# Kernel tuning notes

Hardware: AMD Instinct MI355X
Metric: run time of the kernel (lower is better)

The kernel has to match this reference:

```python
import jax, jax.numpy as jnp
import numpy as np

N = 50000
E = 800000
DIN = 64
DOUT = 64
H = 4
C = DOUT // H
EPS = 1e-5


def setup_inputs() -> dict:
    key = jax.random.key(0)
    ks = jax.random.split(key, 40)
    inp = {}
    inp["x"] = jax.random.normal(ks[0], (N, DIN), jnp.float32)
    inp["edge_index"] = jax.random.randint(ks[1], (2, E), 0, N, dtype=jnp.int32)
    inp["edge_weight"] = jax.random.uniform(ks[2], (E,), jnp.float32)
    inp["edge_attr"] = jax.random.normal(ks[3], (E, 1), jnp.float32)
    k = 4
    for i in range(2):
        din = DIN if i == 0 else DOUT
        s = din ** -0.5
        inp[f"gcn_w{i}"] = jax.random.normal(ks[k], (din, DOUT), jnp.float32) * s; k += 1
        inp[f"gcn_b{i}"] = jnp.zeros((DOUT,), jnp.float32)
        inp[f"res_w{i}"] = jax.random.normal(ks[k], (din, DOUT), jnp.float32) * s; k += 1
        inp[f"res_b{i}"] = jnp.zeros((DOUT,), jnp.float32)
        inp[f"ln_g{i}"] = jnp.ones((DOUT,), jnp.float32)
        inp[f"ln_b{i}"] = jnp.zeros((DOUT,), jnp.float32)
        sg = DOUT ** -0.5
        inp[f"gat_w{i}"] = jax.random.normal(ks[k], (DOUT, H * C), jnp.float32) * sg; k += 1
        inp[f"gat_b{i}"] = jnp.zeros((H * C,), jnp.float32)
        inp[f"att_src{i}"] = jax.random.normal(ks[k], (H, C), jnp.float32) * (C ** -0.5); k += 1
        inp[f"att_dst{i}"] = jax.random.normal(ks[k], (H, C), jnp.float32) * (C ** -0.5); k += 1
        inp[f"att_e{i}"] = jax.random.normal(ks[k], (H, C), jnp.float32) * (C ** -0.5); k += 1
        inp[f"ew_w{i}"] = jax.random.normal(ks[k], (1, H * C), jnp.float32); k += 1
    return inp


def _gcn(x, src0, dst0, ew, W, b):
    n = x.shape[0]
    sl = jnp.arange(n, dtype=src0.dtype)
    src = jnp.concatenate([src0, sl])
    dst = jnp.concatenate([dst0, sl])
    w = jnp.concatenate([ew, jnp.ones((n,), ew.dtype)])  # self-loop weight 1
    deg = jax.ops.segment_sum(w, dst, num_segments=n)
    dinv = jnp.where(deg > 0, jax.lax.rsqrt(deg), 0.0)
    norm = dinv[src] * w * dinv[dst]
    h = x @ W  # [n, DOUT]
    out = jax.ops.segment_sum(h[src] * norm[:, None], dst, num_segments=n)
    return out + b


def _gat(x, src0, dst0, ea, W, b, a_src, a_dst, a_e, We):
    n = x.shape[0]
    sl = jnp.arange(n, dtype=src0.dtype)
    src = jnp.concatenate([src0, sl])
    dst = jnp.concatenate([dst0, sl])
    loop_attr = jnp.broadcast_to(ea.mean(axis=0, keepdims=True), (n, ea.shape[1]))
    ea2 = jnp.concatenate([ea, loop_attr], axis=0)  # fill_value='mean'
    xl = (x @ W).reshape(n, H, C)
    a_s = (xl * a_src).sum(-1)  # [n,H]
    a_d = (xl * a_dst).sum(-1)
    a_ee = ((ea2 @ We).reshape(-1, H, C) * a_e).sum(-1)  # [E2,H]
    alpha = jax.nn.leaky_relu(a_s[src] + a_d[dst] + a_ee, 0.2)
    m = jax.ops.segment_max(alpha, dst, num_segments=n)
    e = jnp.exp(alpha - m[dst])
    s = jax.ops.segment_sum(e, dst, num_segments=n)
    alpha = e / (s[dst] + 1e-16)
    out = jax.ops.segment_sum(xl[src] * alpha[:, :, None], dst, num_segments=n)
    return out.reshape(n, H * C) + b


def _ln(x, g, b):
    mu = x.mean(-1, keepdims=True)
    v = ((x - mu) ** 2).mean(-1, keepdims=True)
    return (x - mu) * jax.lax.rsqrt(v + EPS) * g + b


def reference(x, edge_index, edge_weight, edge_attr,
              gcn_w0, gcn_b0, res_w0, res_b0, ln_g0, ln_b0,
              gat_w0, gat_b0, att_src0, att_dst0, att_e0, ew_w0,
              gcn_w1, gcn_b1, res_w1, res_b1, ln_g1, ln_b1,
              gat_w1, gat_b1, att_src1, att_dst1, att_e1, ew_w1):
    src0, dst0 = edge_index[0], edge_index[1]
    layers = [
        (gcn_w0, gcn_b0, res_w0, res_b0, ln_g0, ln_b0, gat_w0, gat_b0, att_src0, att_dst0, att_e0, ew_w0),
        (gcn_w1, gcn_b1, res_w1, res_b1, ln_g1, ln_b1, gat_w1, gat_b1, att_src1, att_dst1, att_e1, ew_w1),
    ]
    for (gw, gb, rw, rb, lg, lb, Wg, bg, a_s, a_d, a_e, We) in layers:
        residual = x @ rw + rb
        x = jax.nn.silu(_gcn(x, src0, dst0, edge_weight, gw, gb)) + residual
        x = _ln(x, lg, lb)
        x = jax.nn.silu(_gat(x, src0, dst0, edge_attr, Wg, bg, a_s, a_d, a_e, We)) + x
    return x  # down_sample=False -> Identity
```

## Files before the change

### kernel.cpp

```cpp
#include <hip/hip_runtime.h>
#include <hip/hip_fp16.h>

#define NN 50000
#define NE 800000
#define D 64
#define EPS 1e-5f
#define NT 3125
#define NB1 250
#define EPB 3200
#define NBIN 196
#define STOT 49152
#define SBLK 192

typedef unsigned short ushort_t;
typedef unsigned int uint_t;
typedef __attribute__((ext_vector_type(8))) short bf16x8;
typedef __attribute__((ext_vector_type(4))) float f32x4;

__device__ __forceinline__ float wave_sum64(float v) {
#pragma unroll
  for (int m = 1; m <= 32; m <<= 1) v += __shfl_xor(v, m, 64);
  return v;
}
__device__ __forceinline__ float group_sum16(float v) {
#pragma unroll
  for (int m = 1; m <= 8; m <<= 1) v += __shfl_xor(v, m, 64);
  return v;
}
__device__ __forceinline__ float silu_f(float v) { return v / (1.f + __expf(-v)); }
__device__ __forceinline__ float lrelu_f(float v) { return v >= 0.f ? v : 0.2f * v; }
__device__ __forceinline__ ushort_t f2b(float x) {
  unsigned u = __float_as_uint(x);
  return (ushort_t)((u + 0x7FFFu + ((u >> 16) & 1u)) >> 16);
}
__device__ __forceinline__ float b2f(ushort_t u) {
  return __uint_as_float(((unsigned)u) << 16);
}
__device__ __forceinline__ ushort_t f2h(float x) {
  return __half_as_ushort(__float2half_rn(x));
}
__device__ __forceinline__ float h2f(unsigned u) {
  return __half2float(__ushort_as_half((ushort_t)(u & 0xFFFFu)));
}
__device__ __forceinline__ float sel4(float a, float b, float c, float d, int h) {
  float ab = (h & 1) ? b : a;
  float cd = (h & 1) ? d : c;
  return (h & 2) ? cd : ab;
}
__device__ __forceinline__ bf16x8 pack8(float4 a, float4 b) {
  bf16x8 r;
  r[0] = (short)f2b(a.x); r[1] = (short)f2b(a.y);
  r[2] = (short)f2b(a.z); r[3] = (short)f2b(a.w);
  r[4] = (short)f2b(b.x); r[5] = (short)f2b(b.y);
  r[6] = (short)f2b(b.z); r[7] = (short)f2b(b.w);
  return r;
}


__global__ void __launch_bounds__(256) k_hist196(const int* __restrict__ ei,
                                                 int* __restrict__ histG) {
  __shared__ int h[NBIN];
  int blk = blockIdx.x;
  for (int j = threadIdx.x; j < NBIN; j += 256) h[j] = 0;
  __syncthreads();
  int e0 = blk * EPB;
  for (int e = e0 + threadIdx.x; e < e0 + EPB; e += 256)
    atomicAdd(&h[ei[NE + e] >> 8], 1);
  __syncthreads();
  for (int j = threadIdx.x; j < NBIN; j += 256) histG[j * NB1 + blk] = h[j];
}

__global__ void __launch_bounds__(256) k_scanMA(int* __restrict__ histG,
                                                int* __restrict__ bsum) {
  __shared__ int sm[256];
  int j = threadIdx.x;
  int i = blockIdx.x * 256 + j;
  const int TOT = NBIN * NB1;
  int v = (i < TOT) ? histG[i] : 0;
  sm[j] = v;
  __syncthreads();
  for (int off = 1; off < 256; off <<= 1) {
    int t = (j >= off) ? sm[j - off] : 0;
    __syncthreads();
    sm[j] += t;
    __syncthreads();
  }
  if (i < TOT) histG[i] = sm[j] - v;
  if (j == 255) bsum[blockIdx.x] = sm[255];
}

__global__ void __launch_bounds__(256) k_scanMB(int* __restrict__ bsum,
                                                float* __restrict__ scal) {
  __shared__ int sm[256];
  int j = threadIdx.x;
  for (int t = j; t < 1024; t += 256) scal[t] = 0.f;
  int v = (j < SBLK) ? bsum[j] : 0;
  sm[j] = v;
  __syncthreads();
  for (int off = 1; off < 256; off <<= 1) {
    int t = (j >= off) ? sm[j - off] : 0;
    __syncthreads();
    sm[j] += t;
    __syncthreads();
  }
  if (j < SBLK) bsum[j] = sm[j] - v;
}

__global__ void __launch_bounds__(256) k_scanMC(int* __restrict__ histG,
                                                const int* __restrict__ bsum) {
  int i = blockIdx.x * 256 + threadIdx.x;
  const int TOT = NBIN * NB1;
  if (i < TOT) histG[i] += bsum[i >> 8];
}

__global__ void __launch_bounds__(256) k_part(
    const int* __restrict__ ei, const float* __restrict__ ew,
    const float* __restrict__ ea, const int* __restrict__ histG,
    uint2* __restrict__ rectmp, float* __restrict__ scal) {
  __shared__ int cur[NBIN];
  int blk = blockIdx.x;
  for (int j = threadIdx.x; j < NBIN; j += 256) cur[j] = histG[j * NB1 + blk];
  __syncthreads();
  int e0 = blk * EPB;
  float asum = 0.f;
  for (int e = e0 + threadIdx.x; e < e0 + EPB; e += 256) {
    int src = ei[e];
    int dst = ei[NE + e];
    float w = ew[e];
    float a = ea[e];
    asum += a;
    int slot = atomicAdd(&cur[dst >> 8], 1);
    uint2 r;
    r.x = (uint_t)(src & 0xFFFF) | ((uint_t)f2h(w) << 16);
    r.y = (uint_t)(dst & 0xFF) | ((uint_t)f2h(a) << 16);
    rectmp[slot] = r;
  }
  float s = wave_sum64(asum);
  if ((threadIdx.x & 63) == 0) {
    int slot = (blk * 4 + (threadIdx.x >> 6)) & 63;
    atomicAdd(&scal[(size_t)slot * 16], s);
  }
}

__global__ void __launch_bounds__(256) k_sortfin(
    const uint2* __restrict__ rectmp, const int* __restrict__ histG,
    uint2* __restrict__ rec, int* __restrict__ rs) {
  __shared__ int cnt[256], sc[256], cur[256];
  int b = blockIdx.x;
  int t = threadIdx.x;
  int lo = histG[b * NB1];
  int hi = (b == NBIN - 1) ? NE : histG[(b + 1) * NB1];
  cnt[t] = 0;
  __syncthreads();
  for (int e = lo + t; e < hi; e += 256)
    atomicAdd(&cnt[rectmp[e].y & 0xFFu], 1);
  __syncthreads();
  int v = cnt[t];
  sc[t] = v;
  __syncthreads();
  for (int off = 1; off < 256; off <<= 1) {
    int u = (t >= off) ? sc[t - off] : 0;
    __syncthreads();
    sc[t] += u;
    __syncthreads();
  }
  int ex = sc[t] - v;
  int node = b * 256 + t;
  if (node < NN) rs[node] = lo + ex;
  if (b == NBIN - 1 && t == 0) rs[NN] = NE;
  cur[t] = lo + ex;
  __syncthreads();
  for (int e = lo + t; e < hi; e += 256) {
    uint2 r = rectmp[e];
    int dl = (int)(r.y & 0xFFu);
    int slot = atomicAdd(&cur[dl], 1);
    uint_t src = r.x & 0xFFFFu;
    uint2 o;
    o.x = r.x;
    o.y = src | (r.y & 0xFFFF0000u);
    rec[slot] = o;
  }
}

__global__ void k_deg(const uint_t* __restrict__ rec, const int* __restrict__ rs,
                      float* __restrict__ dinv, float* __restrict__ scal) {
  int i = blockIdx.x * blockDim.x + threadIdx.x;
  if (i < NN) {
    float s = 1.f;
    int k1 = rs[i + 1];
    for (int k = rs[i]; k < k1; ++k) s += h2f(rec[2 * k] >> 16);
    dinv[i] = rsqrtf(s);
  }
  if (i == 0) {
    float t = 0.f;
    for (int j = 0; j < 64; ++j) t += scal[(size_t)j * 16];
    scal[1] = t / (float)NE;
  }
}

__global__ void __launch_bounds__(256) k_dual_gemm(
    const float* __restrict__ x, const float* __restrict__ W1,
    const float* __restrict__ W2, const float* __restrict__ b2,
    ushort_t* __restrict__ out1, float* __restrict__ out2) {
  __shared__ ushort_t wf[2 * 2 * 4 * 512];
  for (int e = threadIdx.x; e < 8192; e += 256) {
    int f = e >> 9, r = e & 511;
    int lane = r >> 3, j = r & 7;
    int m = f >> 3, s = (f >> 2) & 1, t = f & 3;
    int k = s * 32 + (lane >> 4) * 8 + j;
    int n = t * 16 + (lane & 15);
    const float* Wm = m ? W2 : W1;
    wf[e] = f2b(Wm[k * D + n]);
  }
  __syncthreads();
  int tile = blockIdx.x * 4 + (threadIdx.x >> 6);
  if (tile >= NT) return;
  int l = threadIdx.x & 63;
  int q = l >> 4, cn = l & 15;
  const float* xr = x + ((size_t)tile * 16 + cn) * D + q * 8;
  float4 xa = *(const float4*)xr;
  float4 xb = *(const float4*)(xr + 4);
  float4 xc = *(const float4*)(xr + 32);
  float4 xd = *(const float4*)(xr + 36);
  bf16x8 a0 = pack8(xa, xb), a1 = pack8(xc, xd);
  f32x4 acc1[4], acc2[4];
#pragma unroll
  for (int t = 0; t < 4; ++t) {
    bf16x8 b10 = *(const bf16x8*)&wf[(0 * 8 + 0 * 4 + t) * 512 + l * 8];
    bf16x8 b11 = *(const bf16x8*)&wf[(0 * 8 + 1 * 4 + t) * 512 + l * 8];
    bf16x8 b20 = *(const bf16x8*)&wf[(1 * 8 + 0 * 4 + t) * 512 + l * 8];
    bf16x8 b21 = *(const bf16x8*)&wf[(1 * 8 + 1 * 4 + t) * 512 + l * 8];
    f32x4 z = {0.f, 0.f, 0.f, 0.f};
    acc1[t] = __builtin_amdgcn_mfma_f32_16x16x32_bf16(a0, b10, z, 0, 0, 0);
    acc1[t] = __builtin_amdgcn_mfma_f32_16x16x32_bf16(a1, b11, acc1[t], 0, 0, 0);
    acc2[t] = __builtin_amdgcn_mfma_f32_16x16x32_bf16(a0, b20, z, 0, 0, 0);
    acc2[t] = __builtin_amdgcn_mfma_f32_16x16x32_bf16(a1, b21, acc2[t], 0, 0, 0);
  }
#pragma unroll
  for (int t = 0; t < 4; ++t) {
    float bb = b2[t * 16 + cn];
#pragma unroll
    for (int r = 0; r < 4; ++r) {
      size_t row = (size_t)tile * 16 + q * 4 + r;
      out1[row * D + t * 16 + cn] = f2b(acc1[t][r]);
      out2[row * D + t * 16 + cn] = acc2[t][r] + bb;
    }
  }
}

__global__ void __launch_bounds__(256) k_gat_node(
    const float* __restrict__ x2, const float* __restrict__ Wg,
    const float* __restrict__ att_src, const float* __restrict__ att_dst,
    const float* __restrict__ We, const float* __restrict__ a_e,
    ushort_t* __restrict__ xl, float* __restrict__ a_s, float* __restrict__ a_d,
    float* __restrict__ wea) {
  __shared__ ushort_t wf[2 * 4 * 512];
  for (int e = threadIdx.x; e < 4096; e += 256) {
    int f = e >> 9, r = e & 511;
    int lane = r >> 3, j = r & 7;
    int s = (f >> 2) & 1, t = f & 3;
    int k = s * 32 + (lane >> 4) * 8 + j;
    int n = t * 16 + (lane & 15);
    wf[e] = f2b(Wg[k * D + n]);
  }
  __syncthreads();
  if (blockIdx.x == 0 && threadIdx.x < 64) {
    int c = threadIdx.x;
    float v = group_sum16(We[c] * a_e[c]);
    if ((c & 15) == 0) wea[c >> 4] = v;
  }
  int tile = blockIdx.x * 4 + (threadIdx.x >> 6);
  if (tile >= NT) return;
  int l = threadIdx.x & 63;
  int q = l >> 4, cn = l & 15;
  const float* xr = x2 + ((size_t)tile * 16 + cn) * D + q * 8;
  float4 xa = *(const float4*)xr;
  float4 xb = *(const float4*)(xr + 4);
  float4 xc = *(const float4*)(xr + 32);
  float4 xd = *(const float4*)(xr + 36);
  bf16x8 a0 = pack8(xa, xb), a1 = pack8(xc, xd);
  f32x4 acc[4];
#pragma unroll
  for (int t = 0; t < 4; ++t) {
    bf16x8 b0 = *(const bf16x8*)&wf[(0 * 4 + t) * 512 + l * 8];
    bf16x8 b1 = *(const bf16x8*)&wf[(1 * 4 + t) * 512 + l * 8];
    f32x4 z = {0.f, 0.f, 0.f, 0.f};
    acc[t] = __builtin_amdgcn_mfma_f32_16x16x32_bf16(a0, b0, z, 0, 0, 0);
    acc[t] = __builtin_amdgcn_mfma_f32_16x16x32_bf16(a1, b1, acc[t], 0, 0, 0);
  }
#pragma unroll
  for (int t = 0; t < 4; ++t) {
    float av = att_src[t * 16 + cn];
    float dv = att_dst[t * 16 + cn];
#pragma unroll
    for (int r = 0; r < 4; ++r) {
      size_t row = (size_t)tile * 16 + q * 4 + r;
      xl[row * D + t * 16 + cn] = f2b(acc[t][r]);
      float vs = group_sum16(acc[t][r] * av);
      float vd = group_sum16(acc[t][r] * dv);
      if (cn == 0) {
        a_s[row * 4 + t] = vs;
        a_d[row * 4 + t] = vd;
      }
    }
  }
}


__global__ void __launch_bounds__(256) k_gcn_agg(
    const ushort_t* __restrict__ h16, const float* __restrict__ res,
    const float* __restrict__ dinv, const int* __restrict__ rs,
    const uint_t* __restrict__ rec,
    const float* __restrict__ gb, const float* __restrict__ lg, const float* __restrict__ lb,
    float* __restrict__ x2, int n) {
  __shared__ int   ss[4][64];
  __shared__ float swt[4][64];
  int w = threadIdx.x >> 6;
  int wv = (blockIdx.x * blockDim.x + threadIdx.x) >> 6;
  int iA = wv * 2;
  if (iA >= n) return;
  int iB = iA + 1;
  int l = threadIdx.x & 63;
  int half = l >> 5, cp = l & 31;
  float diA = dinv[iA], diB = dinv[iB];
  float accA = diA * diA * b2f(h16[(size_t)iA * D + l]);
  float accB = diB * diB * b2f(h16[(size_t)iB * D + l]);
  int kA = rs[iA], kA1 = rs[iA + 1];
  int kB = rs[iB], kB1 = rs[iB + 1];
  while (kA < kA1 || kB < kB1) {
    int cntA = min(32, kA1 - kA);
    int cntB = min(32, kB1 - kB);
    int src = 0; float wn = 0.f;
    if (half == 0) {
      if (cp < cntA) {
        uint_t r = rec[2 * (size_t)(kA + cp)];
        src = (int)(r & 0xFFFFu);
        wn = dinv[src] * h2f(r >> 16) * diA;
      }
    } else {
      if (cp < cntB) {
        uint_t r = rec[2 * (size_t)(kB + cp)];
        src = (int)(r & 0xFFFFu);
        wn = dinv[src] * h2f(r >> 16) * diB;
      }
    }
    ss[w][l] = src;
    swt[w][l] = wn;
    int nm = max(cntA, cntB);
    int j = 0;
    for (; j + 4 <= nm; j += 4) {
      int4 sa = *(const int4*)&ss[w][j];
      int4 sb = *(const int4*)&ss[w][32 + j];
      float4 wa = *(const float4*)&swt[w][j];
      float4 wb = *(const float4*)&swt[w][32 + j];
      float a0 = b2f(h16[(size_t)sa.x * D + l]);
      float b0 = b2f(h16[(size_t)sb.x * D + l]);
      float a1 = b2f(h16[(size_t)sa.y * D + l]);
      float b1 = b2f(h16[(size_t)sb.y * D + l]);
      float a2 = b2f(h16[(size_t)sa.z * D + l]);
      float b2v = b2f(h16[(size_t)sb.z * D + l]);
      float a3 = b2f(h16[(size_t)sa.w * D + l]);
      float b3 = b2f(h16[(size_t)sb.w * D + l]);
      accA = fmaf(wa.x, a0, accA); accB = fmaf(wb.x, b0, accB);
      accA = fmaf(wa.y, a1, accA); accB = fmaf(wb.y, b1, accB);
      accA = fmaf(wa.z, a2, accA); accB = fmaf(wb.z, b2v, accB);
      accA = fmaf(wa.w, a3, accA); accB = fmaf(wb.w, b3, accB);
    }
    for (; j < nm; ++j) {
      int sA = ss[w][j], sB = ss[w][32 + j];
      float wA = swt[w][j], wB = swt[w][32 + j];
      float vA = b2f(h16[(size_t)sA * D + l]);
      float vB = b2f(h16[(size_t)sB * D + l]);
      accA = fmaf(wA, vA, accA);
      accB = fmaf(wB, vB, accB);
    }
    kA += cntA; kB += cntB;
  }
  float gbv = gb[l], lgv = lg[l], lbv = lb[l];
  float x1A = silu_f(accA + gbv) + res[(size_t)iA * D + l];
  float x1B = silu_f(accB + gbv) + res[(size_t)iB * D + l];
  float muA = wave_sum64(x1A) * (1.f / 64.f);
  float muB = wave_sum64(x1B) * (1.f / 64.f);
  float dA = x1A - muA, dB = x1B - muB;
  float varA = wave_sum64(dA * dA) * (1.f / 64.f);
  float varB = wave_sum64(dB * dB) * (1.f / 64.f);
  x2[(size_t)iA * D + l] = dA * rsqrtf(varA + EPS) * lgv + lbv;
  x2[(size_t)iB * D + l] = dB * rsqrtf(varB + EPS) * lgv + lbv;
}

__global__ void __launch_bounds__(256) k_gat_agg(
    const ushort_t* __restrict__ xl16, const float* __restrict__ x2,
    const float* __restrict__ a_s, const float* __restrict__ a_d,
    const int* __restrict__ rs, const uint_t* __restrict__ rec,
    const float* __restrict__ wea, const float* __restrict__ scal,
    const float* __restrict__ bg, float* __restrict__ xout, int n) {
  __shared__ int   ss[4][64];
  __shared__ float el[4][4][68];
  int w = threadIdx.x >> 6;
  int wv = (blockIdx.x * blockDim.x + threadIdx.x) >> 6;
  int iA = wv * 2;
  if (iA >= n) return;
  int iB = iA + 1;
  int l = threadIdx.x & 63;
  int half = l >> 5, cp = l & 31;
  int hh = l >> 4;
  float4 wv4 = *(const float4*)wea;
  float mean_attr = scal[1];
  float we_h = sel4(wv4.x, wv4.y, wv4.z, wv4.w, hh);
  float ad_hA = a_d[(size_t)iA * 4 + hh], as_iA = a_s[(size_t)iA * 4 + hh];
  float ad_hB = a_d[(size_t)iB * 4 + hh], as_iB = a_s[(size_t)iB * 4 + hh];
  float eSA = __expf(lrelu_f(as_iA + ad_hA + mean_attr * we_h));
  float eSB = __expf(lrelu_f(as_iB + ad_hB + mean_attr * we_h));
  float sA = eSA, sB = eSB;
  float accA = eSA * b2f(xl16[(size_t)iA * D + l]);
  float accB = eSB * b2f(xl16[(size_t)iB * D + l]);
  const float* adp = a_d + (size_t)(half ? iB : iA) * 4;
  float4 ad4 = *(const float4*)adp;
  int kA = rs[iA], kA1 = rs[iA + 1];
  int kB = rs[iB], kB1 = rs[iB + 1];
  while (kA < kA1 || kB < kB1) {
    int cntA = min(32, kA1 - kA);
    int cntB = min(32, kB1 - kB);
    int myk = half ? kB : kA;
    int mycnt = half ? cntB : cntA;
    int src = 0;
    float e0v = 0.f, e1v = 0.f, e2v = 0.f, e3v = 0.f;
    if (cp < mycnt) {
      uint_t r = rec[2 * (size_t)(myk + cp) + 1];
      src = (int)(r & 0xFFFFu);
      float ea = h2f(r >> 16);
      float4 as4 = *(const float4*)(a_s + (size_t)src * 4);
      e0v = __expf(lrelu_f(as4.x + fmaf(ea, wv4.x, ad4.x)));
      e1v = __expf(lrelu_f(as4.y + fmaf(ea, wv4.y, ad4.y)));
      e2v = __expf(lrelu_f(as4.z + fmaf(ea, wv4.z, ad4.z)));
      e3v = __expf(lrelu_f(as4.w + fmaf(ea, wv4.w, ad4.w)));
    }
    ss[w][l] = src;
    el[w][0][l] = e0v;
    el[w][1][l] = e1v;
    el[w][2][l] = e2v;
    el[w][3][l] = e3v;
    int nm = max(cntA, cntB);
    int j = 0;
    for (; j + 4 <= nm; j += 4) {
      int4 sa = *(const int4*)&ss[w][j];
      int4 sb = *(const int4*)&ss[w][32 + j];
      float4 ea4 = *(const float4*)&el[w][hh][j];
      float4 eb4 = *(const float4*)&el[w][hh][32 + j];
      float a0 = b2f(xl16[(size_t)sa.x * D + l]);
      float b0 = b2f(xl16[(size_t)sb.x * D + l]);
      float a1 = b2f(xl16[(size_t)sa.y * D + l]);
      float b1 = b2f(xl16[(size_t)sb.y * D + l]);
      float a2 = b2f(xl16[(size_t)sa.z * D + l]);
      float b2v = b2f(xl16[(size_t)sb.z * D + l]);
      float a3 = b2f(xl16[(size_t)sa.w * D + l]);
      float b3 = b2f(xl16[(size_t)sb.w * D + l]);
      accA = fmaf(ea4.x, a0, accA); accB = fmaf(eb4.x, b0, accB);
      accA = fmaf(ea4.y, a1, accA); accB = fmaf(eb4.y, b1, accB);
      accA = fmaf(ea4.z, a2, accA); accB = fmaf(eb4.z, b2v, accB);
      accA = fmaf(ea4.w, a3, accA); accB = fmaf(eb4.w, b3, accB);
      sA += (ea4.x + ea4.y) + (ea4.z + ea4.w);
      sB += (eb4.x + eb4.y) + (eb4.z + eb4.w);
    }
    for (; j < nm; ++j) {
      int srcA = ss[w][j], srcB = ss[w][32 + j];
      float eA = el[w][hh][j], eB = el[w][hh][32 + j];
      float vA = b2f(xl16[(size_t)srcA * D + l]);
      float vB = b2f(xl16[(size_t)srcB * D + l]);
      accA = fmaf(eA, vA, accA);
      accB = fmaf(eB, vB, accB);
      sA += eA; sB += eB;
    }
    kA += cntA; kB += cntB;
  }
  float bgv = bg[l];
  float oA = accA / (sA + 1e-16f) + bgv;
  float oB = accB / (sB + 1e-16f) + bgv;
  xout[(size_t)iA * D + l] = silu_f(oA) + x2[(size_t)iA * D + l];
  xout[(size_t)iB * D + l] = silu_f(oB) + x2[(size_t)iB * D + l];
}


extern "C" void kernel_launch(void* const* d_in, const int* in_sizes, int n_in,
                              void* d_out, int out_size, void* d_ws, size_t ws_size,
                              hipStream_t stream) {
  (void)in_sizes; (void)n_in; (void)out_size; (void)ws_size;
  const float* x  = (const float*)d_in[0];
  const int*   ei = (const int*)d_in[1];
  const float* ew = (const float*)d_in[2];
  const float* ea = (const float*)d_in[3];
  const float* P[2][12];
  for (int l = 0; l < 2; ++l)
    for (int j = 0; j < 12; ++j) P[l][j] = (const float*)d_in[4 + l * 12 + j];

  float* W = (float*)d_ws;
  const size_t o_rs    = 0;
  const size_t o_dinv  = o_rs + NN + 16;
  const size_t o_wea   = o_dinv + NN;
  const size_t o_scal  = o_wea + 16;
  const size_t o_bsum  = o_scal + 1024;
  const size_t o_hist  = o_bsum + 256;
  const size_t o_rec   = o_hist + STOT;
  const size_t o_rtmp  = o_rec + (size_t)NE * 2;
  const size_t o_h16   = o_rtmp + (size_t)NE * 2;
  const size_t o_xl16  = o_h16 + (size_t)NN * D / 2;
  const size_t o_res   = o_xl16 + (size_t)NN * D / 2;
  const size_t o_x2    = o_res + (size_t)NN * D;
  const size_t o_xmid  = o_x2 + (size_t)NN * D;
  const size_t o_as    = o_xmid + (size_t)NN * D;
  const size_t o_ad    = o_as + (size_t)NN * 4;

  int*      rs    = (int*)(W + o_rs);
  float*    dinv  = W + o_dinv;
  float*    wea   = W + o_wea;
  float*    scal  = W + o_scal;
  int*      bsum  = (int*)(W + o_bsum);
  int*      histG = (int*)(W + o_hist);
  uint2*    rec   = (uint2*)(W + o_rec);
  uint2*    rtmp  = (uint2*)(W + o_rtmp);
  ushort_t* h16   = (ushort_t*)(W + o_h16);
  ushort_t* xl16  = (ushort_t*)(W + o_xl16);
  float*    resb  = W + o_res;
  float*    x2b   = W + o_x2;
  float*    xmid  = W + o_xmid;
  float*    asb   = W + o_as;
  float*    adb   = W + o_ad;

  const int B = 256;
  const int gN  = (NN + B - 1) / B;
  const int gN2 = ((NN / 2) * 64 + B - 1) / B;
  const int gMF = (NT + 3) / 4;

  k_hist196<<<NB1, B, 0, stream>>>(ei, histG);
  k_scanMA<<<SBLK, B, 0, stream>>>(histG, bsum);
  k_scanMB<<<1, B, 0, stream>>>(bsum, scal);
  k_scanMC<<<SBLK, B, 0, stream>>>(histG, bsum);
  k_part<<<NB1, B, 0, stream>>>(ei, ew, ea, histG, rtmp, scal);
  k_sortfin<<<NBIN, B, 0, stream>>>(rtmp, histG, rec, rs);
  k_deg<<<gN, B, 0, stream>>>((const uint_t*)rec, rs, dinv, scal);

  const float* xin = x;
  for (int l = 0; l < 2; ++l) {
    float* xout = (l == 0) ? xmid : (float*)d_out;
    k_dual_gemm<<<gMF, B, 0, stream>>>(xin, P[l][0], P[l][2], P[l][3], h16, resb);
    k_gcn_agg<<<gN2, B, 0, stream>>>(h16, resb, dinv, rs, (const uint_t*)rec,
                                     P[l][1], P[l][4], P[l][5], x2b, NN);
    k_gat_node<<<gMF, B, 0, stream>>>(x2b, P[l][6], P[l][8], P[l][9],
                                      P[l][11], P[l][10], xl16, asb, adb, wea);
    k_gat_agg<<<gN2, B, 0, stream>>>(xl16, x2b, asb, adb, rs, (const uint_t*)rec,
                                     wea, scal, P[l][7], xout, NN);
    xin = xout;
  }
}
```

Baseline: 312.0 us.

## Fuse node GEMMs into aggregation epilogues and merge preprocessing kernels

The per-node GEMMs move into the aggregation kernels. The GAT projection runs as an MFMA epilogue of the GCN aggregation, and the next layer's GCN/residual GEMM runs at the end of the GAT aggregation, working on 8-node tiles staged in shared memory. The degree computation is folded into the sort-finalise kernel through shared-memory atomics. The scan is shortened to two passes, the weights are pre-converted to bf16 once, and the histogram runs in the same launch as the first GEMM. This removes several launches and the full-size intermediate reads and writes between GEMM and aggregation. The cost is half-empty MFMA tiles (8 of 16 rows used), extra shared-memory syncs, and more register pressure in the aggregation kernels.

```diff
diff --git a/kernel.cpp b/kernel.cpp
--- a/kernel.cpp
+++ b/kernel.cpp
@@ -22,6 +22,11 @@
   for (int m = 1; m <= 32; m <<= 1) v += __shfl_xor(v, m, 64);
   return v;
 }
+__device__ __forceinline__ int wave_sum64i(int v) {
+#pragma unroll
+  for (int m = 1; m <= 32; m <<= 1) v += __shfl_xor(v, m, 64);
+  return v;
+}
 __device__ __forceinline__ float group_sum16(float v) {
 #pragma unroll
   for (int m = 1; m <= 8; m <<= 1) v += __shfl_xor(v, m, 64);
@@ -56,22 +61,109 @@
   return r;
 }
 
-
-__global__ void __launch_bounds__(256) k_hist196(const int* __restrict__ ei,
-                                                 int* __restrict__ histG) {
-  __shared__ int h[NBIN];
-  int blk = blockIdx.x;
-  for (int j = threadIdx.x; j < NBIN; j += 256) h[j] = 0;
-  __syncthreads();
-  int e0 = blk * EPB;
-  for (int e = e0 + threadIdx.x; e < e0 + EPB; e += 256)
-    atomicAdd(&h[ei[NE + e] >> 8], 1);
-  __syncthreads();
-  for (int j = threadIdx.x; j < NBIN; j += 256) histG[j * NB1 + blk] = h[j];
-}
-
-__global__ void __launch_bounds__(256) k_scanMA(int* __restrict__ histG,
-                                                int* __restrict__ bsum) {
+__global__ void __launch_bounds__(256) k_pre(
+    const int* __restrict__ ei, int* __restrict__ histG,
+    const float* __restrict__ x, const float* __restrict__ W1,
+    const float* __restrict__ W2, const float* __restrict__ b2,
+    ushort_t* __restrict__ out1, float* __restrict__ out2) {
+  __shared__ __align__(16) char smem[16384];
+  if (blockIdx.x < NB1) {
+    int* h = (int*)smem;
+    int blk = blockIdx.x;
+    for (int j = threadIdx.x; j < NBIN; j += 256) h[j] = 0;
+    __syncthreads();
+    int e0 = blk * EPB;
+    for (int e = e0 + threadIdx.x; e < e0 + EPB; e += 256)
+      atomicAdd(&h[ei[NE + e] >> 8], 1);
+    __syncthreads();
+    for (int j = threadIdx.x; j < NBIN; j += 256) histG[j * NB1 + blk] = h[j];
+    return;
+  }
+  ushort_t* wf = (ushort_t*)smem;
+  for (int e = threadIdx.x; e < 8192; e += 256) {
+    int f = e >> 9, r = e & 511;
+    int lane = r >> 3, j = r & 7;
+    int m = f >> 3, s = (f >> 2) & 1, t = f & 3;
+    int k = s * 32 + (lane >> 4) * 8 + j;
+    int n = t * 16 + (lane & 15);
+    const float* Wm = m ? W2 : W1;
+    wf[e] = f2b(Wm[k * D + n]);
+  }
+  __syncthreads();
+  int tile = (blockIdx.x - NB1) * 4 + (threadIdx.x >> 6);
+  if (tile >= NT) return;
+  int l = threadIdx.x & 63;
+  int q = l >> 4, cn = l & 15;
+  const float* xr = x + ((size_t)tile * 16 + cn) * D + q * 8;
+  float4 xa = *(const float4*)xr;
+  float4 xb = *(const float4*)(xr + 4);
+  float4 xc = *(const float4*)(xr + 32);
+  float4 xd = *(const float4*)(xr + 36);
+  bf16x8 a0 = pack8(xa, xb), a1 = pack8(xc, xd);
+  f32x4 acc1[4], acc2[4];
+#pragma unroll
+  for (int t = 0; t < 4; ++t) {
+    bf16x8 b10 = *(const bf16x8*)&wf[(0 * 8 + 0 * 4 + t) * 512 + l * 8];
+    bf16x8 b11 = *(const bf16x8*)&wf[(0 * 8 + 1 * 4 + t) * 512 + l * 8];
+    bf16x8 b20 = *(const bf16x8*)&wf[(1 * 8 + 0 * 4 + t) * 512 + l * 8];
+    bf16x8 b21 = *(const bf16x8*)&wf[(1 * 8 + 1 * 4 + t) * 512 + l * 8];
+    f32x4 z = {0.f, 0.f, 0.f, 0.f};
+    acc1[t] = __builtin_amdgcn_mfma_f32_16x16x32_bf16(a0, b10, z, 0, 0, 0);
+    acc1[t] = __builtin_amdgcn_mfma_f32_16x16x32_bf16(a1, b11, acc1[t], 0, 0, 0);
+    acc2[t] = __builtin_amdgcn_mfma_f32_16x16x32_bf16(a0, b20, z, 0, 0, 0);
+    acc2[t] = __builtin_amdgcn_mfma_f32_16x16x32_bf16(a1, b21, acc2[t], 0, 0, 0);
+  }
+#pragma unroll
+  for (int t = 0; t < 4; ++t) {
+    float bb = b2[t * 16 + cn];
+#pragma unroll
+    for (int r = 0; r < 4; ++r) {
+      size_t row = (size_t)tile * 16 + q * 4 + r;
+      out1[row * D + t * 16 + cn] = f2b(acc1[t][r]);
+      out2[row * D + t * 16 + cn] = acc2[t][r] + bb;
+    }
+  }
+}
+
+__global__ void __launch_bounds__(256) k_scanA(
+    int* __restrict__ histG, int* __restrict__ bsum, float* __restrict__ scal,
+    const float* __restrict__ Wg0, const float* __restrict__ Wg1,
+    const float* __restrict__ W11, const float* __restrict__ W21,
+    const float* __restrict__ We0, const float* __restrict__ ae0,
+    const float* __restrict__ We1, const float* __restrict__ ae1,
+    ushort_t* __restrict__ wg16, ushort_t* __restrict__ wd16,
+    float* __restrict__ wea2) {
+  if (blockIdx.x == SBLK) {
+    int tid = threadIdx.x;
+    for (int t = tid; t < 1024; t += 256) scal[t] = 0.f;
+    for (int e = tid; e < 4096; e += 256) {
+      int f = e >> 9, r = e & 511;
+      int lane = r >> 3, j = r & 7;
+      int s = (f >> 2) & 1, t = f & 3;
+      int k = s * 32 + (lane >> 4) * 8 + j;
+      int n = t * 16 + (lane & 15);
+      wg16[e] = f2b(Wg0[k * D + n]);
+      wg16[4096 + e] = f2b(Wg1[k * D + n]);
+    }
+    for (int e = tid; e < 8192; e += 256) {
+      int f = e >> 9, r = e & 511;
+      int lane = r >> 3, j = r & 7;
+      int m = f >> 3, s = (f >> 2) & 1, t = f & 3;
+      int k = s * 32 + (lane >> 4) * 8 + j;
+      int n = t * 16 + (lane & 15);
+      const float* Wm = m ? W21 : W11;
+      wd16[e] = f2b(Wm[k * D + n]);
+    }
+    if (tid < 64) {
+      float v = group_sum16(We0[tid] * ae0[tid]);
+      if ((tid & 15) == 0) wea2[tid >> 4] = v;
+    } else if (tid < 128) {
+      int c = tid - 64;
+      float v = group_sum16(We1[c] * ae1[c]);
+      if ((c & 15) == 0) wea2[4 + (c >> 4)] = v;
+    }
+    return;
+  }
   __shared__ int sm[256];
   int j = threadIdx.x;
   int i = blockIdx.x * 256 + j;
@@ -89,28 +181,17 @@
   if (j == 255) bsum[blockIdx.x] = sm[255];
 }
 
-__global__ void __launch_bounds__(256) k_scanMB(int* __restrict__ bsum,
-                                                float* __restrict__ scal) {
-  __shared__ int sm[256];
-  int j = threadIdx.x;
-  for (int t = j; t < 1024; t += 256) scal[t] = 0.f;
-  int v = (j < SBLK) ? bsum[j] : 0;
-  sm[j] = v;
-  __syncthreads();
-  for (int off = 1; off < 256; off <<= 1) {
-    int t = (j >= off) ? sm[j - off] : 0;
-    __syncthreads();
-    sm[j] += t;
-    __syncthreads();
-  }
-  if (j < SBLK) bsum[j] = sm[j] - v;
-}
-
-__global__ void __launch_bounds__(256) k_scanMC(int* __restrict__ histG,
-                                                const int* __restrict__ bsum) {
-  int i = blockIdx.x * 256 + threadIdx.x;
-  const int TOT = NBIN * NB1;
-  if (i < TOT) histG[i] += bsum[i >> 8];
+__global__ void __launch_bounds__(256) k_scanC(int* __restrict__ histG,
+                                               const int* __restrict__ bsum) {
+  __shared__ int ws4[4];
+  int t = threadIdx.x;
+  int v = (t < (int)blockIdx.x) ? bsum[t] : 0;
+  v = wave_sum64i(v);
+  if ((t & 63) == 0) ws4[t >> 6] = v;
+  __syncthreads();
+  int prefix = ws4[0] + ws4[1] + ws4[2] + ws4[3];
+  int i = blockIdx.x * 256 + t;
+  if (i < NBIN * NB1) histG[i] += prefix;
 }
 
 __global__ void __launch_bounds__(256) k_part(
@@ -142,15 +223,18 @@
   }
 }
 
-__global__ void __launch_bounds__(256) k_sortfin(
+__global__ void __launch_bounds__(256) k_sfin(
     const uint2* __restrict__ rectmp, const int* __restrict__ histG,
-    uint2* __restrict__ rec, int* __restrict__ rs) {
+    uint2* __restrict__ rec, int* __restrict__ rs,
+    float* __restrict__ dinv, float* __restrict__ scal) {
   __shared__ int cnt[256], sc[256], cur[256];
+  __shared__ float wsum[256];
   int b = blockIdx.x;
   int t = threadIdx.x;
   int lo = histG[b * NB1];
   int hi = (b == NBIN - 1) ? NE : histG[(b + 1) * NB1];
   cnt[t] = 0;
+  wsum[t] = 0.f;
   __syncthreads();
   for (int e = lo + t; e < hi; e += 256)
     atomicAdd(&cnt[rectmp[e].y & 0xFFu], 1);
@@ -174,153 +258,40 @@
     uint2 r = rectmp[e];
     int dl = (int)(r.y & 0xFFu);
     int slot = atomicAdd(&cur[dl], 1);
+    atomicAdd(&wsum[dl], h2f(r.x >> 16));
     uint_t src = r.x & 0xFFFFu;
     uint2 o;
     o.x = r.x;
     o.y = src | (r.y & 0xFFFF0000u);
     rec[slot] = o;
   }
-}
-
-__global__ void k_deg(const uint_t* __restrict__ rec, const int* __restrict__ rs,
-                      float* __restrict__ dinv, float* __restrict__ scal) {
-  int i = blockIdx.x * blockDim.x + threadIdx.x;
-  if (i < NN) {
-    float s = 1.f;
-    int k1 = rs[i + 1];
-    for (int k = rs[i]; k < k1; ++k) s += h2f(rec[2 * k] >> 16);
-    dinv[i] = rsqrtf(s);
-  }
-  if (i == 0) {
-    float t = 0.f;
-    for (int j = 0; j < 64; ++j) t += scal[(size_t)j * 16];
-    scal[1] = t / (float)NE;
-  }
-}
-
-__global__ void __launch_bounds__(256) k_dual_gemm(
-    const float* __restrict__ x, const float* __restrict__ W1,
-    const float* __restrict__ W2, const float* __restrict__ b2,
-    ushort_t* __restrict__ out1, float* __restrict__ out2) {
-  __shared__ ushort_t wf[2 * 2 * 4 * 512];
-  for (int e = threadIdx.x; e < 8192; e += 256) {
-    int f = e >> 9, r = e & 511;
-    int lane = r >> 3, j = r & 7;
-    int m = f >> 3, s = (f >> 2) & 1, t = f & 3;
-    int k = s * 32 + (lane >> 4) * 8 + j;
-    int n = t * 16 + (lane & 15);
-    const float* Wm = m ? W2 : W1;
-    wf[e] = f2b(Wm[k * D + n]);
-  }
-  __syncthreads();
-  int tile = blockIdx.x * 4 + (threadIdx.x >> 6);
-  if (tile >= NT) return;
-  int l = threadIdx.x & 63;
-  int q = l >> 4, cn = l & 15;
-  const float* xr = x + ((size_t)tile * 16 + cn) * D + q * 8;
-  float4 xa = *(const float4*)xr;
-  float4 xb = *(const float4*)(xr + 4);
-  float4 xc = *(const float4*)(xr + 32);
-  float4 xd = *(const float4*)(xr + 36);
-  bf16x8 a0 = pack8(xa, xb), a1 = pack8(xc, xd);
-  f32x4 acc1[4], acc2[4];
-#pragma unroll
-  for (int t = 0; t < 4; ++t) {
-    bf16x8 b10 = *(const bf16x8*)&wf[(0 * 8 + 0 * 4 + t) * 512 + l * 8];
-    bf16x8 b11 = *(const bf16x8*)&wf[(0 * 8 + 1 * 4 + t) * 512 + l * 8];
-    bf16x8 b20 = *(const bf16x8*)&wf[(1 * 8 + 0 * 4 + t) * 512 + l * 8];
-    bf16x8 b21 = *(const bf16x8*)&wf[(1 * 8 + 1 * 4 + t) * 512 + l * 8];
-    f32x4 z = {0.f, 0.f, 0.f, 0.f};
-    acc1[t] = __builtin_amdgcn_mfma_f32_16x16x32_bf16(a0, b10, z, 0, 0, 0);
-    acc1[t] = __builtin_amdgcn_mfma_f32_16x16x32_bf16(a1, b11, acc1[t], 0, 0, 0);
-    acc2[t] = __builtin_amdgcn_mfma_f32_16x16x32_bf16(a0, b20, z, 0, 0, 0);
-    acc2[t] = __builtin_amdgcn_mfma_f32_16x16x32_bf16(a1, b21, acc2[t], 0, 0, 0);
-  }
-#pragma unroll
-  for (int t = 0; t < 4; ++t) {
-    float bb = b2[t * 16 + cn];
-#pragma unroll
-    for (int r = 0; r < 4; ++r) {
-      size_t row = (size_t)tile * 16 + q * 4 + r;
-      out1[row * D + t * 16 + cn] = f2b(acc1[t][r]);
-      out2[row * D + t * 16 + cn] = acc2[t][r] + bb;
-    }
-  }
-}
-
-__global__ void __launch_bounds__(256) k_gat_node(
-    const float* __restrict__ x2, const float* __restrict__ Wg,
-    const float* __restrict__ att_src, const float* __restrict__ att_dst,
-    const float* __restrict__ We, const float* __restrict__ a_e,
-    ushort_t* __restrict__ xl, float* __restrict__ a_s, float* __restrict__ a_d,
-    float* __restrict__ wea) {
-  __shared__ ushort_t wf[2 * 4 * 512];
-  for (int e = threadIdx.x; e < 4096; e += 256) {
-    int f = e >> 9, r = e & 511;
-    int lane = r >> 3, j = r & 7;
-    int s = (f >> 2) & 1, t = f & 3;
-    int k = s * 32 + (lane >> 4) * 8 + j;
-    int n = t * 16 + (lane & 15);
-    wf[e] = f2b(Wg[k * D + n]);
-  }
-  __syncthreads();
-  if (blockIdx.x == 0 && threadIdx.x < 64) {
-    int c = threadIdx.x;
-    float v = group_sum16(We[c] * a_e[c]);
-    if ((c & 15) == 0) wea[c >> 4] = v;
-  }
-  int tile = blockIdx.x * 4 + (threadIdx.x >> 6);
-  if (tile >= NT) return;
-  int l = threadIdx.x & 63;
-  int q = l >> 4, cn = l & 15;
-  const float* xr = x2 + ((size_t)tile * 16 + cn) * D + q * 8;
-  float4 xa = *(const float4*)xr;
-  float4 xb = *(const float4*)(xr + 4);
-  float4 xc = *(const float4*)(xr + 32);
-  float4 xd = *(const float4*)(xr + 36);
-  bf16x8 a0 = pack8(xa, xb), a1 = pack8(xc, xd);
-  f32x4 acc[4];
-#pragma unroll
-  for (int t = 0; t < 4; ++t) {
-    bf16x8 b0 = *(const bf16x8*)&wf[(0 * 4 + t) * 512 + l * 8];
-    bf16x8 b1 = *(const bf16x8*)&wf[(1 * 4 + t) * 512 + l * 8];
-    f32x4 z = {0.f, 0.f, 0.f, 0.f};
-    acc[t] = __builtin_amdgcn_mfma_f32_16x16x32_bf16(a0, b0, z, 0, 0, 0);
-    acc[t] = __builtin_amdgcn_mfma_f32_16x16x32_bf16(a1, b1, acc[t], 0, 0, 0);
-  }
-#pragma unroll
-  for (int t = 0; t < 4; ++t) {
-    float av = att_src[t * 16 + cn];
-    float dv = att_dst[t * 16 + cn];
-#pragma unroll
-    for (int r = 0; r < 4; ++r) {
-      size_t row = (size_t)tile * 16 + q * 4 + r;
-      xl[row * D + t * 16 + cn] = f2b(acc[t][r]);
-      float vs = group_sum16(acc[t][r] * av);
-      float vd = group_sum16(acc[t][r] * dv);
-      if (cn == 0) {
-        a_s[row * 4 + t] = vs;
-        a_d[row * 4 + t] = vd;
-      }
-    }
-  }
-}
-
-
-__global__ void __launch_bounds__(256) k_gcn_agg(
+  __syncthreads();
+  if (node < NN) dinv[node] = rsqrtf(1.f + wsum[t]);
+  if (b == 0 && t == 0) {
+    float s = 0.f;
+    for (int j = 0; j < 64; ++j) s += scal[(size_t)j * 16];
+    scal[1] = s / (float)NE;
+  }
+}
+
+__global__ void __launch_bounds__(256) k_gcn_gat(
     const ushort_t* __restrict__ h16, const float* __restrict__ res,
     const float* __restrict__ dinv, const int* __restrict__ rs,
     const uint_t* __restrict__ rec,
-    const float* __restrict__ gb, const float* __restrict__ lg, const float* __restrict__ lb,
-    float* __restrict__ x2, int n) {
-  __shared__ int   ss[4][64];
+    const float* __restrict__ gb, const float* __restrict__ lg,
+    const float* __restrict__ lb,
+    const ushort_t* __restrict__ wg, const float* __restrict__ att_src,
+    const float* __restrict__ att_dst,
+    float* __restrict__ x2, ushort_t* __restrict__ xl,
+    float* __restrict__ a_s, float* __restrict__ a_d) {
+  __shared__ int ss[4][64];
   __shared__ float swt[4][64];
+  __shared__ __align__(16) ushort_t xt[16][72];
   int w = threadIdx.x >> 6;
-  int wv = (blockIdx.x * blockDim.x + threadIdx.x) >> 6;
-  int iA = wv * 2;
-  if (iA >= n) return;
+  int l = threadIdx.x & 63;
+  int base = blockIdx.x * 8;
+  int iA = base + 2 * w;
   int iB = iA + 1;
-  int l = threadIdx.x & 63;
   int half = l >> 5, cp = l & 31;
   float diA = dinv[iA], diB = dinv[iB];
   float accA = diA * diA * b2f(h16[(size_t)iA * D + l]);
@@ -384,22 +355,59 @@
   float dA = x1A - muA, dB = x1B - muB;
   float varA = wave_sum64(dA * dA) * (1.f / 64.f);
   float varB = wave_sum64(dB * dB) * (1.f / 64.f);
-  x2[(size_t)iA * D + l] = dA * rsqrtf(varA + EPS) * lgv + lbv;
-  x2[(size_t)iB * D + l] = dB * rsqrtf(varB + EPS) * lgv + lbv;
-}
-
-__global__ void __launch_bounds__(256) k_gat_agg(
+  float oA = dA * rsqrtf(varA + EPS) * lgv + lbv;
+  float oB = dB * rsqrtf(varB + EPS) * lgv + lbv;
+  x2[(size_t)iA * D + l] = oA;
+  x2[(size_t)iB * D + l] = oB;
+  xt[2 * w][l] = f2b(oA);
+  xt[2 * w + 1][l] = f2b(oB);
+  {
+    ushort_t* xz = &xt[8][0];
+    for (int e = threadIdx.x; e < 8 * 72; e += 256) xz[e] = 0;
+  }
+  __syncthreads();
+  int t = w;
+  int q = l >> 4, cn = l & 15;
+  bf16x8 a0 = *(const bf16x8*)&xt[cn][q * 8];
+  bf16x8 a1 = *(const bf16x8*)&xt[cn][q * 8 + 32];
+  bf16x8 b0 = *(const bf16x8*)&wg[(size_t)((0 * 4 + t) * 512 + l * 8)];
+  bf16x8 b1 = *(const bf16x8*)&wg[(size_t)((1 * 4 + t) * 512 + l * 8)];
+  f32x4 z = {0.f, 0.f, 0.f, 0.f};
+  f32x4 acc = __builtin_amdgcn_mfma_f32_16x16x32_bf16(a0, b0, z, 0, 0, 0);
+  acc = __builtin_amdgcn_mfma_f32_16x16x32_bf16(a1, b1, acc, 0, 0, 0);
+  if (q < 2) {
+    float av = att_src[t * 16 + cn];
+    float dv = att_dst[t * 16 + cn];
+#pragma unroll
+    for (int r = 0; r < 4; ++r) {
+      size_t row = (size_t)base + q * 4 + r;
+      xl[row * D + t * 16 + cn] = f2b(acc[r]);
+      float vs = group_sum16(acc[r] * av);
+      float vd = group_sum16(acc[r] * dv);
+      if (cn == 0) {
+        a_s[row * 4 + t] = vs;
+        a_d[row * 4 + t] = vd;
+      }
+    }
+  }
+}
+
+template <int FUSE>
+__global__ void __launch_bounds__(256) k_gat_fin(
     const ushort_t* __restrict__ xl16, const float* __restrict__ x2,
     const float* __restrict__ a_s, const float* __restrict__ a_d,
     const int* __restrict__ rs, const uint_t* __restrict__ rec,
     const float* __restrict__ wea, const float* __restrict__ scal,
-    const float* __restrict__ bg, float* __restrict__ xout, int n) {
-  __shared__ int   ss[4][64];
+    const float* __restrict__ bg,
+    const ushort_t* __restrict__ wd, const float* __restrict__ b2,
+    ushort_t* __restrict__ out1, float* __restrict__ out2,
+    float* __restrict__ xout) {
+  __shared__ int ss[4][64];
   __shared__ float el[4][4][68];
+  __shared__ __align__(16) ushort_t xt[16][72];
   int w = threadIdx.x >> 6;
-  int wv = (blockIdx.x * blockDim.x + threadIdx.x) >> 6;
-  int iA = wv * 2;
-  if (iA >= n) return;
+  int base = blockIdx.x * 8;
+  int iA = base + 2 * w;
   int iB = iA + 1;
   int l = threadIdx.x & 63;
   int half = l >> 5, cp = l & 31;
@@ -476,8 +484,43 @@
   float bgv = bg[l];
   float oA = accA / (sA + 1e-16f) + bgv;
   float oB = accB / (sB + 1e-16f) + bgv;
-  xout[(size_t)iA * D + l] = silu_f(oA) + x2[(size_t)iA * D + l];
-  xout[(size_t)iB * D + l] = silu_f(oB) + x2[(size_t)iB * D + l];
+  float vA = silu_f(oA) + x2[(size_t)iA * D + l];
+  float vB = silu_f(oB) + x2[(size_t)iB * D + l];
+  if (FUSE) {
+    xt[2 * w][l] = f2b(vA);
+    xt[2 * w + 1][l] = f2b(vB);
+    {
+      ushort_t* xz = &xt[8][0];
+      for (int e = threadIdx.x; e < 8 * 72; e += 256) xz[e] = 0;
+    }
+    __syncthreads();
+    int t = w;
+    int q = l >> 4, cn = l & 15;
+    bf16x8 a0 = *(const bf16x8*)&xt[cn][q * 8];
+    bf16x8 a1 = *(const bf16x8*)&xt[cn][q * 8 + 32];
+#pragma unroll
+    for (int m = 0; m < 2; ++m) {
+      bf16x8 b0 = *(const bf16x8*)&wd[(size_t)((m * 8 + 0 * 4 + t) * 512 + l * 8)];
+      bf16x8 b1 = *(const bf16x8*)&wd[(size_t)((m * 8 + 1 * 4 + t) * 512 + l * 8)];
+      f32x4 z = {0.f, 0.f, 0.f, 0.f};
+      f32x4 acc = __builtin_amdgcn_mfma_f32_16x16x32_bf16(a0, b0, z, 0, 0, 0);
+      acc = __builtin_amdgcn_mfma_f32_16x16x32_bf16(a1, b1, acc, 0, 0, 0);
+      if (q < 2) {
+        float bb = (m == 1) ? b2[t * 16 + cn] : 0.f;
+#pragma unroll
+        for (int r = 0; r < 4; ++r) {
+          size_t row = (size_t)base + q * 4 + r;
+          if (m == 0)
+            out1[row * D + t * 16 + cn] = f2b(acc[r]);
+          else
+            out2[row * D + t * 16 + cn] = acc[r] + bb;
+        }
+      }
+    }
+  } else {
+    xout[(size_t)iA * D + l] = vA;
+    xout[(size_t)iB * D + l] = vB;
+  }
 }
 
 
@@ -506,13 +549,14 @@
   const size_t o_xl16  = o_h16 + (size_t)NN * D / 2;
   const size_t o_res   = o_xl16 + (size_t)NN * D / 2;
   const size_t o_x2    = o_res + (size_t)NN * D;
-  const size_t o_xmid  = o_x2 + (size_t)NN * D;
-  const size_t o_as    = o_xmid + (size_t)NN * D;
+  const size_t o_as    = o_x2 + (size_t)NN * D;
   const size_t o_ad    = o_as + (size_t)NN * 4;
+  const size_t o_wg16  = o_ad + (size_t)NN * 4;
+  const size_t o_wd16  = o_wg16 + 4096;
 
   int*      rs    = (int*)(W + o_rs);
   float*    dinv  = W + o_dinv;
-  float*    wea   = W + o_wea;
+  float*    wea2  = W + o_wea;
   float*    scal  = W + o_scal;
   int*      bsum  = (int*)(W + o_bsum);
   int*      histG = (int*)(W + o_hist);
@@ -522,33 +566,37 @@
   ushort_t* xl16  = (ushort_t*)(W + o_xl16);
   float*    resb  = W + o_res;
   float*    x2b   = W + o_x2;
-  float*    xmid  = W + o_xmid;
   float*    asb   = W + o_as;
   float*    adb   = W + o_ad;
+  ushort_t* wg16  = (ushort_t*)(W + o_wg16);
+  ushort_t* wd16  = (ushort_t*)(W + o_wd16);
 
   const int B = 256;
-  const int gN  = (NN + B - 1) / B;
-  const int gN2 = ((NN / 2) * 64 + B - 1) / B;
-  const int gMF = (NT + 3) / 4;
-
-  k_hist196<<<NB1, B, 0, stream>>>(ei, histG);
-  k_scanMA<<<SBLK, B, 0, stream>>>(histG, bsum);
-  k_scanMB<<<1, B, 0, stream>>>(bsum, scal);
-  k_scanMC<<<SBLK, B, 0, stream>>>(histG, bsum);
+  const int gPre = NB1 + (NT + 3) / 4;
+  const int gN2  = NN / 8;
+
+  k_pre<<<gPre, B, 0, stream>>>(ei, histG, x, P[0][0], P[0][2], P[0][3], h16, resb);
+  k_scanA<<<SBLK + 1, B, 0, stream>>>(histG, bsum, scal,
+                                      P[0][6], P[1][6], P[1][0], P[1][2],
+                                      P[0][11], P[0][10], P[1][11], P[1][10],
+                                      wg16, wd16, wea2);
+  k_scanC<<<SBLK, B, 0, stream>>>(histG, bsum);
   k_part<<<NB1, B, 0, stream>>>(ei, ew, ea, histG, rtmp, scal);
-  k_sortfin<<<NBIN, B, 0, stream>>>(rtmp, histG, rec, rs);
-  k_deg<<<gN, B, 0, stream>>>((const uint_t*)rec, rs, dinv, scal);
-
-  const float* xin = x;
-  for (int l = 0; l < 2; ++l) {
-    float* xout = (l == 0) ? xmid : (float*)d_out;
-    k_dual_gemm<<<gMF, B, 0, stream>>>(xin, P[l][0], P[l][2], P[l][3], h16, resb);
-    k_gcn_agg<<<gN2, B, 0, stream>>>(h16, resb, dinv, rs, (const uint_t*)rec,
-                                     P[l][1], P[l][4], P[l][5], x2b, NN);
-    k_gat_node<<<gMF, B, 0, stream>>>(x2b, P[l][6], P[l][8], P[l][9],
-                                      P[l][11], P[l][10], xl16, asb, adb, wea);
-    k_gat_agg<<<gN2, B, 0, stream>>>(xl16, x2b, asb, adb, rs, (const uint_t*)rec,
-                                     wea, scal, P[l][7], xout, NN);
-    xin = xout;
-  }
-}
+  k_sfin<<<NBIN, B, 0, stream>>>(rtmp, histG, rec, rs, dinv, scal);
+
+  k_gcn_gat<<<gN2, B, 0, stream>>>(h16, resb, dinv, rs, (const uint_t*)rec,
+                                   P[0][1], P[0][4], P[0][5],
+                                   wg16, P[0][8], P[0][9],
+                                   x2b, xl16, asb, adb);
+  k_gat_fin<1><<<gN2, B, 0, stream>>>(xl16, x2b, asb, adb, rs, (const uint_t*)rec,
+                                      wea2, scal, P[0][7],
+                                      wd16, P[1][3], h16, resb, nullptr);
+  k_gcn_gat<<<gN2, B, 0, stream>>>(h16, resb, dinv, rs, (const uint_t*)rec,
+                                   P[1][1], P[1][4], P[1][5],
+                                   wg16 + 4096, P[1][8], P[1][9],
+                                   x2b, xl16, asb, adb);
+  k_gat_fin<0><<<gN2, B, 0, stream>>>(xl16, x2b, asb, adb, rs, (const uint_t*)rec,
+                                      wea2 + 4, scal, P[1][7],
+                                      nullptr, nullptr, nullptr, nullptr,
+                                      (float*)d_out);
+}
```

Result: faster. 297.0 us (-4.8%).
